# Optimization experiments

Hardware: AMD Instinct MI355X
Metric: run time of the kernel (lower is better)

## Reference

```python
import jax, jax.numpy as jnp
import numpy as np

B, N, IN_DIM, HID, EMB, E = 64, 2048, 128, 256, 64, 4194304
TOTAL = B * N


def _init(key, shape, fan_in):
    return jax.random.normal(key, shape, jnp.float32) / np.sqrt(fan_in).astype(np.float32)


def setup_inputs() -> dict:
    key = jax.random.key(0)
    ks = jax.random.split(key, 9)
    x = jax.random.normal(ks[0], (TOTAL, IN_DIM), jnp.float32)
    src = jax.random.randint(ks[1], (E,), 0, TOTAL)
    dst = jax.random.randint(ks[2], (E,), 0, TOTAL)
    return {
        "x": x,
        "src": src,
        "dst": dst,
        "num_nodes": TOTAL,
        "nodes_per_graph": N,
        "w_lin": _init(ks[3], (IN_DIM, HID), IN_DIM),
        "b_lin": jnp.zeros((HID,), jnp.float32),
        "w_c0": _init(ks[4], (HID, HID), HID),
        "b_c0": jnp.zeros((HID,), jnp.float32),
        "w_c1": _init(ks[5], (HID, HID), HID),
        "b_c1": jnp.zeros((HID,), jnp.float32),
        "w_emb": _init(ks[6], (HID, EMB), HID),
        "b_emb": jnp.zeros((EMB,), jnp.float32),
    }


def reference(x, src, dst, num_nodes, nodes_per_graph,
              w_lin, b_lin, w_c0, b_c0, w_c1, b_c1, w_emb, b_emb):
    # DGL GraphConv norm='both': deg clamped to min 1, symmetric normalization
    ones = jnp.ones(src.shape, x.dtype)
    out_deg = jax.ops.segment_sum(ones, src, num_segments=num_nodes)
    in_deg = jax.ops.segment_sum(ones, dst, num_segments=num_nodes)
    out_norm = jnp.maximum(out_deg, 1.0) ** -0.5  # [num_nodes]
    in_norm = jnp.maximum(in_deg, 1.0) ** -0.5

    def graph_conv(h, W, b):
        hs = h * out_norm[:, None]                                   # pre-norm by out-degree
        agg = jax.ops.segment_sum(hs[src], dst, num_segments=num_nodes)  # SpMM: sum messages
        return (agg * in_norm[:, None]) @ W + b                      # post-norm, then weight

    h = jax.nn.relu(x @ w_lin + b_lin)          # [total, HID]
    h = jax.nn.relu(graph_conv(h, w_c0, b_c0))  # residual=False for agg_style='node'
    h = jax.nn.relu(graph_conv(h, w_c1, b_c1))
    # agent node 0 of each graph in the batch: indices 0, N, 2N, ...
    agent = h[jnp.arange(0, num_nodes, nodes_per_graph)]  # [B, HID]
    return agent @ w_emb + b_emb                          # [B, EMB]
```

## Files before the change

kernel.cpp:

```cpp
#include <hip/hip_runtime.h>
#include <hip/hip_bf16.h>

#define TOTAL_N   131072
#define NEDGE     4194304
#define NPG       2048
#define IN_DIM_K  128
#define HID_K     256
#define EMB_K     64
#define NAGENT    64

#define F1CAP     4096
#define APACK     128
#define BCAP      96

#define G1        256
#define EPB1      (NEDGE / G1)
#define HWORDS    (TOTAL_N / 8)

#define SELB      256
#define EPB       (NEDGE / SELB)


#define ZERO_SPAN 589824

typedef float f32x4 __attribute__((ext_vector_type(4)));
typedef short bf16x8 __attribute__((ext_vector_type(8)));

__device__ inline unsigned short f2bf(float f) {
    unsigned int u = __float_as_uint(f);
    return (unsigned short)((u + 0x7FFFu + ((u >> 16) & 1u)) >> 16);
}

__global__ __launch_bounds__(1024) void k_outdeg_e0(
    const int* __restrict__ src, const int* __restrict__ dst,
    unsigned int* __restrict__ partial,
    int* __restrict__ flag,
    int* __restrict__ e0pack, int* __restrict__ e0cnt)
{
    __shared__ unsigned int hist[HWORDS];
    int t = threadIdx.x;
    #pragma unroll
    for (int i = 0; i < HWORDS / 1024; i++) hist[t + i * 1024] = 0u;
    __syncthreads();

    int ebase = blockIdx.x * EPB1;
    const int4* s4 = (const int4*)(src + ebase);
    const int4* d4 = (const int4*)(dst + ebase);
    #pragma unroll
    for (int i = 0; i < EPB1 / 4096; i++) {
        int4 sv = s4[i * 1024 + t];
        int4 dv = d4[i * 1024 + t];
        int ss[4] = {sv.x, sv.y, sv.z, sv.w};
        int dd[4] = {dv.x, dv.y, dv.z, dv.w};
        #pragma unroll
        for (int j = 0; j < 4; j++) {
            int s = ss[j], d = dd[j];
            atomicAdd(&hist[s >> 3], 1u << ((s & 7) * 4));
            if ((d & (NPG - 1)) == 0) {
                flag[s] = 1;
                int a = d >> 11;
                int slot = atomicAdd(&e0cnt[a], 1);
                if (slot < APACK) e0pack[a * APACK + slot] = s;
            }
        }
    }
    __syncthreads();
    unsigned int* pout = partial + blockIdx.x * HWORDS;
    #pragma unroll
    for (int i = 0; i < HWORDS / 1024; i++) pout[t + i * 1024] = hist[t + i * 1024];
}

__global__ __launch_bounds__(1024) void k_auxred(
    const int* __restrict__ flag, int* __restrict__ loc,
    int* __restrict__ counters, unsigned long long* __restrict__ bitmap,
    const unsigned int* __restrict__ partial, unsigned int* __restrict__ out_deg,
    const float* __restrict__ wlin, unsigned short* __restrict__ wswz)
{
    int b = blockIdx.x;
    int t = threadIdx.x;
    if (b < 128) {
        __shared__ int cnt, gbase;
        if (t == 0) cnt = 0;
        __syncthreads();
        int v = b * 1024 + t;
        int f = flag[v];
        unsigned long long m = __ballot(f != 0);
        if ((t & 63) == 0) bitmap[v >> 6] = m;
        int p = -1;
        if (f) p = atomicAdd(&cnt, 1);
        __syncthreads();
        if (t == 0) gbase = cnt ? atomicAdd(&counters[1], cnt) : 0;
        __syncthreads();
        int l = -1;
        if (p >= 0) { int id = gbase + p; if (id < F1CAP) l = id; }
        loc[v] = l;
    } else if (b < 256) {
        __shared__ unsigned int redE[8][128], redO[8][128];
        int wl = t & 127, gs = t >> 7;
        int w = (b - 128) * 128 + wl;
        unsigned int accE = 0, accO = 0;
        #pragma unroll 8
        for (int i = 0; i < 32; i++) {
            unsigned int v = partial[(gs * 32 + i) * HWORDS + w];
            accE += v & 0x0F0F0F0Fu;
            accO += (v >> 4) & 0x0F0F0F0Fu;
        }
        redE[gs][wl] = accE;
        redO[gs][wl] = accO;
        __syncthreads();
        if (gs == 0) {
            unsigned int sE = 0, sO = 0;
            #pragma unroll
            for (int j = 0; j < 8; j++) { sE += redE[j][wl]; sO += redO[j][wl]; }
            uint4 lo = make_uint4(sE & 255u, sO & 255u, (sE >> 8) & 255u, (sO >> 8) & 255u);
            uint4 hi = make_uint4((sE >> 16) & 255u, (sO >> 16) & 255u, (sE >> 24) & 255u, (sO >> 24) & 255u);
            ((uint4*)(out_deg + 8 * w))[0] = lo;
            ((uint4*)(out_deg + 8 * w))[1] = hi;
        }
    } else {
        int g = (b - 256) * 1024 + t;
        int lane = g & 63, ct = (g >> 6) & 15, kt = g >> 10;
        int colbase = ct * 16 + (lane & 15);
        int kbase = kt * 32 + (lane >> 4) * 8;
        unsigned short o[8];
        #pragma unroll
        for (int i = 0; i < 8; i++) o[i] = f2bf(wlin[(kbase + i) * HID_K + colbase]);
        *(ushort4*)(wswz + g * 8)     = make_ushort4(o[0], o[1], o[2], o[3]);
        *(ushort4*)(wswz + g * 8 + 4) = make_ushort4(o[4], o[5], o[6], o[7]);
    }
}

__global__ __launch_bounds__(1024) void k_e1_select(
    const int* __restrict__ src, const int* __restrict__ dst,
    const int* __restrict__ loc, const unsigned int* __restrict__ bitmap,
    int* __restrict__ inF1, int* __restrict__ es_bucket)
{
    __shared__ unsigned int bm[TOTAL_N / 32];
    int t = threadIdx.x;
    ((uint4*)bm)[t] = ((const uint4*)bitmap)[t];
    __syncthreads();

    int ebase = blockIdx.x * EPB;
    const int4* d4p = (const int4*)(dst + ebase);
    #pragma unroll
    for (int i = 0; i < EPB / 4096; i++) {
        int4 d4 = d4p[i * 1024 + t];
        int eidx = ebase + (i * 1024 + t) * 4;
        int dd[4] = {d4.x, d4.y, d4.z, d4.w};
        #pragma unroll
        for (int j = 0; j < 4; j++) {
            int d = dd[j];
            if ((bm[d >> 5] >> (d & 31)) & 1u) {
                int l = loc[d];
                if (l >= 0) {
                    int slot = atomicAdd(&inF1[l], 1);
                    if (slot < BCAP) es_bucket[l * BCAP + slot] = src[eidx + j];
                }
            }
        }
    }
}

__global__ __launch_bounds__(256) void k_h0agg(
    const float* __restrict__ x, const unsigned short* __restrict__ wswz,
    const float* __restrict__ blin, const int* __restrict__ es_bucket,
    const unsigned int* __restrict__ out_deg, const int* __restrict__ inF1,
    const int* __restrict__ counters, float* __restrict__ agg1)
{
    __shared__ unsigned short A[32][136];
    __shared__ float escs[32];
    __shared__ int rsrc[32];

    int nF1 = min(counters[1], F1CAP);
    int l = blockIdx.x;
    if (l >= nF1) return;
    int cnt = min(inF1[l], BCAP);
    int t = threadIdx.x;
    int lane = t & 63, wq = t >> 6;
    int cbase = lane & 15, rgrp = (lane >> 4) * 4;

    float bj[4];
    #pragma unroll
    for (int n = 0; n < 4; n++) bj[n] = blin[wq * 64 + n * 16 + cbase];

    float colacc[4] = {0.f, 0.f, 0.f, 0.f};
    int ntile = (cnt + 31) >> 5;

    for (int ti = 0; ti < ntile; ti++) {
        __syncthreads();
        if (t < 32) {
            int r = ti * 32 + t;
            int s = (r < cnt) ? es_bucket[l * BCAP + r] : -1;
            rsrc[t] = s;
            escs[t] = (s >= 0) ? rsqrtf((float)max((int)out_deg[s], 1)) : 0.f;
        }
        __syncthreads();
        #pragma unroll
        for (int i = 0; i < 4; i++) {
            int idx = t + i * 256;
            int r = idx >> 5, q = idx & 31;
            int s = rsrc[r];
            float4 v = make_float4(0.f, 0.f, 0.f, 0.f);
            if (s >= 0) v = ((const float4*)(x + (long long)s * IN_DIM_K))[q];
            ushort4 h;
            h.x = f2bf(v.x); h.y = f2bf(v.y); h.z = f2bf(v.z); h.w = f2bf(v.w);
            *(ushort4*)&A[r][q * 4] = h;
        }
        __syncthreads();

        f32x4 acc[2][4];
        #pragma unroll
        for (int m = 0; m < 2; m++)
            #pragma unroll
            for (int n = 0; n < 4; n++) acc[m][n] = (f32x4){0.f, 0.f, 0.f, 0.f};

        const unsigned short* Ab = &A[0][0];
        #pragma unroll
        for (int kt = 0; kt < 4; kt++) {
            bf16x8 a0 = *(const bf16x8*)(Ab + ((lane & 15) * 136 + kt * 32 + (lane >> 4) * 8));
            bf16x8 a1 = *(const bf16x8*)(Ab + (((lane & 15) + 16) * 136 + kt * 32 + (lane >> 4) * 8));
            #pragma unroll
            for (int n = 0; n < 4; n++) {
                bf16x8 bf = *(const bf16x8*)(wswz + ((kt * 16 + wq * 4 + n) * 64 + lane) * 8);
                acc[0][n] = __builtin_amdgcn_mfma_f32_16x16x32_bf16(a0, bf, acc[0][n], 0, 0, 0);
                acc[1][n] = __builtin_amdgcn_mfma_f32_16x16x32_bf16(a1, bf, acc[1][n], 0, 0, 0);
            }
        }

        #pragma unroll
        for (int n = 0; n < 4; n++) {
            float part = 0.f;
            #pragma unroll
            for (int m = 0; m < 2; m++)
                #pragma unroll
                for (int j = 0; j < 4; j++) {
                    int row = m * 16 + rgrp + j;
                    part += fmaxf(acc[m][n][j] + bj[n], 0.f) * escs[row];
                }
            part += __shfl_xor(part, 16);
            part += __shfl_xor(part, 32);
            colacc[n] += part;
        }
    }

    if (lane < 16) {
        #pragma unroll
        for (int n = 0; n < 4; n++)
            agg1[l * HID_K + wq * 64 + n * 16 + lane] = colacc[n];
    }
}

__global__ __launch_bounds__(256) void k_h1(
    const float* __restrict__ agg1, const float* __restrict__ wc0,
    const float* __restrict__ bc0,
    const int* __restrict__ inF1,
    const int* __restrict__ counters, float* __restrict__ h1)
{
    __shared__ float as[16][HID_K];
    __shared__ float ns[16];

    int nF1 = min(counters[1], F1CAP);
    int base = blockIdx.x * 16;
    if (base >= nF1) return;
    int t = threadIdx.x;

    if (t < 16) {
        int l = base + t;
        ns[t] = (l < nF1) ? rsqrtf((float)max(inF1[l], 1)) : 0.f;
    }
    __syncthreads();

    #pragma unroll
    for (int i = 0; i < 4; i++) {
        int idx = t + i * 256;
        int e = idx >> 6;
        int q = idx & 63;
        int l = base + e;
        float4 v = make_float4(0.f, 0.f, 0.f, 0.f);
        if (l < nF1) v = ((const float4*)(agg1 + (long long)l * HID_K))[q];
        float sc = ns[e];
        v.x *= sc; v.y *= sc; v.z *= sc; v.w *= sc;
        ((float4*)as[e])[q] = v;
    }
    __syncthreads();

    float acc[16];
    #pragma unroll
    for (int e = 0; e < 16; e++) acc[e] = 0.f;

    int j = t;
    for (int k = 0; k < HID_K; k += 4) {
        float w0 = wc0[(k + 0) * HID_K + j];
        float w1 = wc0[(k + 1) * HID_K + j];
        float w2 = wc0[(k + 2) * HID_K + j];
        float w3 = wc0[(k + 3) * HID_K + j];
        #pragma unroll
        for (int e = 0; e < 16; e++) {
            float4 av = *(const float4*)&as[e][k];
            acc[e] = fmaf(av.x, w0, acc[e]);
            acc[e] = fmaf(av.y, w1, acc[e]);
            acc[e] = fmaf(av.z, w2, acc[e]);
            acc[e] = fmaf(av.w, w3, acc[e]);
        }
    }

    float bj = bc0[j];
    #pragma unroll
    for (int e = 0; e < 16; e++) {
        int l = base + e;
        if (l < nF1) h1[l * HID_K + j] = fmaxf(acc[e] + bj, 0.f);
    }
}

__global__ __launch_bounds__(256) void k_final(
    const int* __restrict__ e0pack, const int* __restrict__ e0cnt,
    const int* __restrict__ loc, const unsigned int* __restrict__ out_deg,
    const float* __restrict__ h1,
    const float* __restrict__ wc1, const float* __restrict__ bc1,
    const float* __restrict__ wemb, const float* __restrict__ bemb,
    float* __restrict__ out)
{
    __shared__ float a_s[HID_K];
    __shared__ float h2[HID_K];
    __shared__ int   ls[APACK];
    __shared__ float scs[APACK];
    int a = blockIdx.x;
    int t = threadIdx.x;

    int n0 = e0cnt[a];
    int ne = min(n0, APACK);
    if (t < ne) {
        int s = e0pack[a * APACK + t];
        int l = loc[s];
        ls[t] = l;
        scs[t] = (l >= 0) ? rsqrtf((float)max((int)out_deg[s], 1)) : 0.f;
    }
    __syncthreads();

    float acc = 0.f;
    for (int i = 0; i < ne; i++) {
        int l = ls[i];
        if (l >= 0) acc = fmaf(scs[i], h1[(long long)l * HID_K + t], acc);
    }
    a_s[t] = acc * rsqrtf((float)max(n0, 1));
    __syncthreads();

    float h = 0.f;
    for (int k = 0; k < HID_K; k++)
        h = fmaf(a_s[k], wc1[k * HID_K + t], h);
    h2[t] = fmaxf(h + bc1[t], 0.f);
    __syncthreads();

    if (t < EMB_K) {
        float o = bemb[t];
        for (int k = 0; k < HID_K; k++)
            o = fmaf(h2[k], wemb[k * EMB_K + t], o);
        out[a * EMB_K + t] = o;
    }
}

extern "C" void kernel_launch(void* const* d_in, const int* in_sizes, int n_in,
                              void* d_out, int out_size, void* d_ws, size_t ws_size,
                              hipStream_t stream)
{
    const float* x    = (const float*)d_in[0];
    const int*   src  = (const int*)d_in[1];
    const int*   dst  = (const int*)d_in[2];
    const float* wlin = (const float*)d_in[5];
    const float* blin = (const float*)d_in[6];
    const float* wc0  = (const float*)d_in[7];
    const float* bc0  = (const float*)d_in[8];
    const float* wc1  = (const float*)d_in[9];
    const float* bc1  = (const float*)d_in[10];
    const float* wemb = (const float*)d_in[11];
    const float* bemb = (const float*)d_in[12];
    float* out = (float*)d_out;

    char* ws = (char*)d_ws;
    int*                counters  = (int*)(ws + 0);
    int*                inF1      = (int*)(ws + 1024);
    int*                e0cnt     = (int*)(ws + 17408);
    int*                flag      = (int*)(ws + 65536);
    int*                loc       = (int*)(ws + 589824);
    int*                e0pack    = (int*)(ws + 1114112);
    int*                es_bucket = (int*)(ws + 1146880);
    unsigned int*       out_deg   = (unsigned int*)(ws + 2719744);
    unsigned short*     wswz      = (unsigned short*)(ws + 3244032);
    float*              h1        = (float*)(ws + 3309568);
    float*              agg1      = (float*)(ws + 7503872);
    unsigned int*       partial   = (unsigned int*)(ws + 11698176);
    unsigned long long* bitmap    = (unsigned long long*)(ws + 28475392);

    hipMemsetAsync(ws, 0, ZERO_SPAN, stream);

    k_outdeg_e0<<<G1, 1024, 0, stream>>>(src, dst, partial, flag, e0pack, e0cnt);
    k_auxred<<<260, 1024, 0, stream>>>(flag, loc, counters, bitmap,
                                       partial, out_deg, wlin, wswz);
    k_e1_select<<<SELB, 1024, 0, stream>>>(src, dst, loc,
                                           (const unsigned int*)bitmap,
                                           inF1, es_bucket);
    k_h0agg<<<F1CAP, 256, 0, stream>>>(x, wswz, blin, es_bucket, out_deg,
                                       inF1, counters, agg1);
    k_h1<<<F1CAP / 16, 256, 0, stream>>>(agg1, wc0, bc0, inF1, counters, h1);
    k_final<<<NAGENT, 256, 0, stream>>>(e0pack, e0cnt, loc, out_deg, h1,
                                        wc1, bc1, wemb, bemb, out);
}
```

Before: 119.7 us.

## Fuse h0 aggregation with first GraphConv weight; replace flag array with atomic bitmap

Merges the per-node aggregation kernel and the wc0 matmul kernel into one kernel that handles 8 frontier nodes per block. The normalized aggregates stay in shared memory instead of round-tripping through global memory, and the bf16 weight fragments are held in registers across nodes. Separately, the int flag array is replaced by a bitmap built with atomicOr, which shrinks the memset from about 590KB to about 34KB and removes a ballot pass. The trade-offs are serial work inside each block, a launch of only 512 blocks, and more register pressure from the 16 held fragments.

```diff
diff --git a/kernel.cpp b/kernel.cpp
--- a/kernel.cpp
+++ b/kernel.cpp
@@ -12,6 +12,7 @@
 #define F1CAP     4096
 #define APACK     128
 #define BCAP      96
+#define NL        8
 
 #define G1        256
 #define EPB1      (NEDGE / G1)
@@ -21,7 +22,7 @@
 #define EPB       (NEDGE / SELB)
 
 
-#define ZERO_SPAN 589824
+#define ZERO_SPAN 34048
 
 typedef float f32x4 __attribute__((ext_vector_type(4)));
 typedef short bf16x8 __attribute__((ext_vector_type(8)));
@@ -34,7 +35,7 @@
 __global__ __launch_bounds__(1024) void k_outdeg_e0(
     const int* __restrict__ src, const int* __restrict__ dst,
     unsigned int* __restrict__ partial,
-    int* __restrict__ flag,
+    unsigned int* __restrict__ bitmap,
     int* __restrict__ e0pack, int* __restrict__ e0cnt)
 {
     __shared__ unsigned int hist[HWORDS];
@@ -57,7 +58,7 @@
             int s = ss[j], d = dd[j];
             atomicAdd(&hist[s >> 3], 1u << ((s & 7) * 4));
             if ((d & (NPG - 1)) == 0) {
-                flag[s] = 1;
+                atomicOr(&bitmap[s >> 5], 1u << (s & 31));
                 int a = d >> 11;
                 int slot = atomicAdd(&e0cnt[a], 1);
                 if (slot < APACK) e0pack[a * APACK + slot] = s;
@@ -71,8 +72,8 @@
 }
 
 __global__ __launch_bounds__(1024) void k_auxred(
-    const int* __restrict__ flag, int* __restrict__ loc,
-    int* __restrict__ counters, unsigned long long* __restrict__ bitmap,
+    const unsigned int* __restrict__ bitmap, int* __restrict__ loc,
+    int* __restrict__ counters,
     const unsigned int* __restrict__ partial, unsigned int* __restrict__ out_deg,
     const float* __restrict__ wlin, unsigned short* __restrict__ wswz)
 {
@@ -83,9 +84,7 @@
         if (t == 0) cnt = 0;
         __syncthreads();
         int v = b * 1024 + t;
-        int f = flag[v];
-        unsigned long long m = __ballot(f != 0);
-        if ((t & 63) == 0) bitmap[v >> 6] = m;
+        int f = (bitmap[v >> 5] >> (v & 31)) & 1u;
         int p = -1;
         if (f) p = atomicAdd(&cnt, 1);
         __syncthreads();
@@ -161,133 +160,111 @@
     }
 }
 
-__global__ __launch_bounds__(256) void k_h0agg(
+__global__ __launch_bounds__(256) void k_h0h1(
     const float* __restrict__ x, const unsigned short* __restrict__ wswz,
     const float* __restrict__ blin, const int* __restrict__ es_bucket,
     const unsigned int* __restrict__ out_deg, const int* __restrict__ inF1,
-    const int* __restrict__ counters, float* __restrict__ agg1)
+    const int* __restrict__ counters,
+    const float* __restrict__ wc0, const float* __restrict__ bc0,
+    float* __restrict__ h1)
 {
     __shared__ unsigned short A[32][136];
+    __shared__ float as[NL][HID_K];
     __shared__ float escs[32];
     __shared__ int rsrc[32];
 
     int nF1 = min(counters[1], F1CAP);
-    int l = blockIdx.x;
-    if (l >= nF1) return;
-    int cnt = min(inF1[l], BCAP);
+    int base = blockIdx.x * NL;
+    if (base >= nF1) return;
     int t = threadIdx.x;
     int lane = t & 63, wq = t >> 6;
     int cbase = lane & 15, rgrp = (lane >> 4) * 4;
 
+    bf16x8 bfrag[4][4];
+    #pragma unroll
+    for (int kt = 0; kt < 4; kt++)
+        #pragma unroll
+        for (int n = 0; n < 4; n++)
+            bfrag[kt][n] = *(const bf16x8*)(wswz + ((kt * 16 + wq * 4 + n) * 64 + lane) * 8);
+
     float bj[4];
     #pragma unroll
     for (int n = 0; n < 4; n++) bj[n] = blin[wq * 64 + n * 16 + cbase];
 
-    float colacc[4] = {0.f, 0.f, 0.f, 0.f};
-    int ntile = (cnt + 31) >> 5;
-
-    for (int ti = 0; ti < ntile; ti++) {
-        __syncthreads();
-        if (t < 32) {
-            int r = ti * 32 + t;
-            int s = (r < cnt) ? es_bucket[l * BCAP + r] : -1;
-            rsrc[t] = s;
-            escs[t] = (s >= 0) ? rsqrtf((float)max((int)out_deg[s], 1)) : 0.f;
-        }
-        __syncthreads();
-        #pragma unroll
-        for (int i = 0; i < 4; i++) {
-            int idx = t + i * 256;
-            int r = idx >> 5, q = idx & 31;
-            int s = rsrc[r];
-            float4 v = make_float4(0.f, 0.f, 0.f, 0.f);
-            if (s >= 0) v = ((const float4*)(x + (long long)s * IN_DIM_K))[q];
-            ushort4 h;
-            h.x = f2bf(v.x); h.y = f2bf(v.y); h.z = f2bf(v.z); h.w = f2bf(v.w);
-            *(ushort4*)&A[r][q * 4] = h;
-        }
-        __syncthreads();
-
-        f32x4 acc[2][4];
-        #pragma unroll
-        for (int m = 0; m < 2; m++)
-            #pragma unroll
-            for (int n = 0; n < 4; n++) acc[m][n] = (f32x4){0.f, 0.f, 0.f, 0.f};
-
-        const unsigned short* Ab = &A[0][0];
-        #pragma unroll
-        for (int kt = 0; kt < 4; kt++) {
-            bf16x8 a0 = *(const bf16x8*)(Ab + ((lane & 15) * 136 + kt * 32 + (lane >> 4) * 8));
-            bf16x8 a1 = *(const bf16x8*)(Ab + (((lane & 15) + 16) * 136 + kt * 32 + (lane >> 4) * 8));
-            #pragma unroll
-            for (int n = 0; n < 4; n++) {
-                bf16x8 bf = *(const bf16x8*)(wswz + ((kt * 16 + wq * 4 + n) * 64 + lane) * 8);
-                acc[0][n] = __builtin_amdgcn_mfma_f32_16x16x32_bf16(a0, bf, acc[0][n], 0, 0, 0);
-                acc[1][n] = __builtin_amdgcn_mfma_f32_16x16x32_bf16(a1, bf, acc[1][n], 0, 0, 0);
-            }
-        }
-
-        #pragma unroll
-        for (int n = 0; n < 4; n++) {
-            float part = 0.f;
+    for (int r = 0; r < NL; r++) {
+        int l = base + r;
+        int cnt = (l < nF1) ? min(inF1[l], BCAP) : 0;
+        float colacc[4] = {0.f, 0.f, 0.f, 0.f};
+        int ntile = (cnt + 31) >> 5;
+
+        for (int ti = 0; ti < ntile; ti++) {
+            __syncthreads();
+            if (t < 32) {
+                int rr = ti * 32 + t;
+                int s = (rr < cnt) ? es_bucket[l * BCAP + rr] : -1;
+                rsrc[t] = s;
+                escs[t] = (s >= 0) ? rsqrtf((float)max((int)out_deg[s], 1)) : 0.f;
+            }
+            __syncthreads();
+            #pragma unroll
+            for (int i = 0; i < 4; i++) {
+                int idx = t + i * 256;
+                int rr = idx >> 5, q = idx & 31;
+                int s = rsrc[rr];
+                float4 v = make_float4(0.f, 0.f, 0.f, 0.f);
+                if (s >= 0) v = ((const float4*)(x + (long long)s * IN_DIM_K))[q];
+                ushort4 h;
+                h.x = f2bf(v.x); h.y = f2bf(v.y); h.z = f2bf(v.z); h.w = f2bf(v.w);
+                *(ushort4*)&A[rr][q * 4] = h;
+            }
+            __syncthreads();
+
+            f32x4 acc[2][4];
             #pragma unroll
             for (int m = 0; m < 2; m++)
                 #pragma unroll
-                for (int j = 0; j < 4; j++) {
-                    int row = m * 16 + rgrp + j;
-                    part += fmaxf(acc[m][n][j] + bj[n], 0.f) * escs[row];
+                for (int n = 0; n < 4; n++) acc[m][n] = (f32x4){0.f, 0.f, 0.f, 0.f};
+
+            const unsigned short* Ab = &A[0][0];
+            #pragma unroll
+            for (int kt = 0; kt < 4; kt++) {
+                bf16x8 a0 = *(const bf16x8*)(Ab + ((lane & 15) * 136 + kt * 32 + (lane >> 4) * 8));
+                bf16x8 a1 = *(const bf16x8*)(Ab + (((lane & 15) + 16) * 136 + kt * 32 + (lane >> 4) * 8));
+                #pragma unroll
+                for (int n = 0; n < 4; n++) {
+                    acc[0][n] = __builtin_amdgcn_mfma_f32_16x16x32_bf16(a0, bfrag[kt][n], acc[0][n], 0, 0, 0);
+                    acc[1][n] = __builtin_amdgcn_mfma_f32_16x16x32_bf16(a1, bfrag[kt][n], acc[1][n], 0, 0, 0);
                 }
-            part += __shfl_xor(part, 16);
-            part += __shfl_xor(part, 32);
-            colacc[n] += part;
-        }
-    }
-
-    if (lane < 16) {
-        #pragma unroll
-        for (int n = 0; n < 4; n++)
-            agg1[l * HID_K + wq * 64 + n * 16 + lane] = colacc[n];
-    }
-}
-
-__global__ __launch_bounds__(256) void k_h1(
-    const float* __restrict__ agg1, const float* __restrict__ wc0,
-    const float* __restrict__ bc0,
-    const int* __restrict__ inF1,
-    const int* __restrict__ counters, float* __restrict__ h1)
-{
-    __shared__ float as[16][HID_K];
-    __shared__ float ns[16];
-
-    int nF1 = min(counters[1], F1CAP);
-    int base = blockIdx.x * 16;
-    if (base >= nF1) return;
-    int t = threadIdx.x;
-
-    if (t < 16) {
-        int l = base + t;
-        ns[t] = (l < nF1) ? rsqrtf((float)max(inF1[l], 1)) : 0.f;
-    }
-    __syncthreads();
-
-    #pragma unroll
-    for (int i = 0; i < 4; i++) {
-        int idx = t + i * 256;
-        int e = idx >> 6;
-        int q = idx & 63;
-        int l = base + e;
-        float4 v = make_float4(0.f, 0.f, 0.f, 0.f);
-        if (l < nF1) v = ((const float4*)(agg1 + (long long)l * HID_K))[q];
-        float sc = ns[e];
-        v.x *= sc; v.y *= sc; v.z *= sc; v.w *= sc;
-        ((float4*)as[e])[q] = v;
-    }
-    __syncthreads();
-
-    float acc[16];
-    #pragma unroll
-    for (int e = 0; e < 16; e++) acc[e] = 0.f;
-
+            }
+
+            #pragma unroll
+            for (int n = 0; n < 4; n++) {
+                float part = 0.f;
+                #pragma unroll
+                for (int m = 0; m < 2; m++)
+                    #pragma unroll
+                    for (int j = 0; j < 4; j++) {
+                        int row = m * 16 + rgrp + j;
+                        part += fmaxf(acc[m][n][j] + bj[n], 0.f) * escs[row];
+                    }
+                part += __shfl_xor(part, 16);
+                part += __shfl_xor(part, 32);
+                colacc[n] += part;
+            }
+        }
+
+        float ns = (l < nF1) ? rsqrtf((float)max(inF1[l], 1)) : 0.f;
+        if (lane < 16) {
+            #pragma unroll
+            for (int n = 0; n < 4; n++)
+                as[r][wq * 64 + n * 16 + lane] = colacc[n] * ns;
+        }
+    }
+    __syncthreads();
+
+    float acc8[NL];
+    #pragma unroll
+    for (int e = 0; e < NL; e++) acc8[e] = 0.f;
     int j = t;
     for (int k = 0; k < HID_K; k += 4) {
         float w0 = wc0[(k + 0) * HID_K + j];
@@ -295,20 +272,19 @@
         float w2 = wc0[(k + 2) * HID_K + j];
         float w3 = wc0[(k + 3) * HID_K + j];
         #pragma unroll
-        for (int e = 0; e < 16; e++) {
+        for (int e = 0; e < NL; e++) {
             float4 av = *(const float4*)&as[e][k];
-            acc[e] = fmaf(av.x, w0, acc[e]);
-            acc[e] = fmaf(av.y, w1, acc[e]);
-            acc[e] = fmaf(av.z, w2, acc[e]);
-            acc[e] = fmaf(av.w, w3, acc[e]);
-        }
-    }
-
-    float bj = bc0[j];
-    #pragma unroll
-    for (int e = 0; e < 16; e++) {
+            acc8[e] = fmaf(av.x, w0, acc8[e]);
+            acc8[e] = fmaf(av.y, w1, acc8[e]);
+            acc8[e] = fmaf(av.z, w2, acc8[e]);
+            acc8[e] = fmaf(av.w, w3, acc8[e]);
+        }
+    }
+    float bcj = bc0[j];
+    #pragma unroll
+    for (int e = 0; e < NL; e++) {
         int l = base + e;
-        if (l < nF1) h1[l * HID_K + j] = fmaxf(acc[e] + bj, 0.f);
+        if (l < nF1) h1[(long long)l * HID_K + j] = fmaxf(acc8[e] + bcj, 0.f);
     }
 }
 
@@ -377,31 +353,27 @@
     float* out = (float*)d_out;
 
     char* ws = (char*)d_ws;
-    int*                counters  = (int*)(ws + 0);
-    int*                inF1      = (int*)(ws + 1024);
-    int*                e0cnt     = (int*)(ws + 17408);
-    int*                flag      = (int*)(ws + 65536);
-    int*                loc       = (int*)(ws + 589824);
-    int*                e0pack    = (int*)(ws + 1114112);
-    int*                es_bucket = (int*)(ws + 1146880);
-    unsigned int*       out_deg   = (unsigned int*)(ws + 2719744);
-    unsigned short*     wswz      = (unsigned short*)(ws + 3244032);
-    float*              h1        = (float*)(ws + 3309568);
-    float*              agg1      = (float*)(ws + 7503872);
-    unsigned int*       partial   = (unsigned int*)(ws + 11698176);
-    unsigned long long* bitmap    = (unsigned long long*)(ws + 28475392);
+    int*            counters  = (int*)(ws + 0);
+    int*            inF1      = (int*)(ws + 1024);
+    int*            e0cnt     = (int*)(ws + 17408);
+    unsigned int*   bitmap    = (unsigned int*)(ws + 17664);
+    int*            loc       = (int*)(ws + 65536);
+    int*            e0pack    = (int*)(ws + 589824);
+    int*            es_bucket = (int*)(ws + 622592);
+    unsigned int*   out_deg   = (unsigned int*)(ws + 2195456);
+    unsigned short* wswz      = (unsigned short*)(ws + 2719744);
+    float*          h1        = (float*)(ws + 2785280);
+    unsigned int*   partial   = (unsigned int*)(ws + 6979584);
 
     hipMemsetAsync(ws, 0, ZERO_SPAN, stream);
 
-    k_outdeg_e0<<<G1, 1024, 0, stream>>>(src, dst, partial, flag, e0pack, e0cnt);
-    k_auxred<<<260, 1024, 0, stream>>>(flag, loc, counters, bitmap,
+    k_outdeg_e0<<<G1, 1024, 0, stream>>>(src, dst, partial, bitmap, e0pack, e0cnt);
+    k_auxred<<<260, 1024, 0, stream>>>(bitmap, loc, counters,
                                        partial, out_deg, wlin, wswz);
-    k_e1_select<<<SELB, 1024, 0, stream>>>(src, dst, loc,
-                                           (const unsigned int*)bitmap,
+    k_e1_select<<<SELB, 1024, 0, stream>>>(src, dst, loc, bitmap,
                                            inF1, es_bucket);
-    k_h0agg<<<F1CAP, 256, 0, stream>>>(x, wswz, blin, es_bucket, out_deg,
-                                       inF1, counters, agg1);
-    k_h1<<<F1CAP / 16, 256, 0, stream>>>(agg1, wc0, bc0, inF1, counters, h1);
+    k_h0h1<<<F1CAP / NL, 256, 0, stream>>>(x, wswz, blin, es_bucket, out_deg,
+                                           inF1, counters, wc0, bc0, h1);
     k_final<<<NAGENT, 256, 0, stream>>>(e0pack, e0cnt, loc, out_deg, h1,
                                         wc1, bc1, wemb, bemb, out);
 }
```

Measured after the change: 118.3 us. No clear change (-1.2%).

## Replace flag array with atomic bitmap and gather all tiles up front in h0agg

Applied to the files above, without the earlier changes.

The per-node int flag array is replaced by a 16 KB bitmap that k_outdeg_e0 sets with atomicOr. This shrinks the memset from about 576 KB to about 33 KB and removes the ballot pass in k_auxred. In k_h0agg, all up to three 32-row tiles of x are gathered into shared memory in one phase before the MFMA loop, which removes the per-tile syncs and lets more gather loads be in flight at once. The cost is global atomics on the bitmap and about three times the shared memory per block, which may lower occupancy.

```diff
diff --git a/kernel.cpp b/kernel.cpp
--- a/kernel.cpp
+++ b/kernel.cpp
@@ -21,7 +21,7 @@
 #define EPB       (NEDGE / SELB)
 
 
-#define ZERO_SPAN 589824
+#define ZERO_SPAN 34048
 
 typedef float f32x4 __attribute__((ext_vector_type(4)));
 typedef short bf16x8 __attribute__((ext_vector_type(8)));
@@ -34,7 +34,7 @@
 __global__ __launch_bounds__(1024) void k_outdeg_e0(
     const int* __restrict__ src, const int* __restrict__ dst,
     unsigned int* __restrict__ partial,
-    int* __restrict__ flag,
+    unsigned int* __restrict__ bitmap,
     int* __restrict__ e0pack, int* __restrict__ e0cnt)
 {
     __shared__ unsigned int hist[HWORDS];
@@ -57,7 +57,7 @@
             int s = ss[j], d = dd[j];
             atomicAdd(&hist[s >> 3], 1u << ((s & 7) * 4));
             if ((d & (NPG - 1)) == 0) {
-                flag[s] = 1;
+                atomicOr(&bitmap[s >> 5], 1u << (s & 31));
                 int a = d >> 11;
                 int slot = atomicAdd(&e0cnt[a], 1);
                 if (slot < APACK) e0pack[a * APACK + slot] = s;
@@ -71,8 +71,8 @@
 }
 
 __global__ __launch_bounds__(1024) void k_auxred(
-    const int* __restrict__ flag, int* __restrict__ loc,
-    int* __restrict__ counters, unsigned long long* __restrict__ bitmap,
+    const unsigned int* __restrict__ bitmap, int* __restrict__ loc,
+    int* __restrict__ counters,
     const unsigned int* __restrict__ partial, unsigned int* __restrict__ out_deg,
     const float* __restrict__ wlin, unsigned short* __restrict__ wswz)
 {
@@ -83,9 +83,7 @@
         if (t == 0) cnt = 0;
         __syncthreads();
         int v = b * 1024 + t;
-        int f = flag[v];
-        unsigned long long m = __ballot(f != 0);
-        if ((t & 63) == 0) bitmap[v >> 6] = m;
+        int f = (bitmap[v >> 5] >> (v & 31)) & 1u;
         int p = -1;
         if (f) p = atomicAdd(&cnt, 1);
         __syncthreads();
@@ -167,54 +165,52 @@
     const unsigned int* __restrict__ out_deg, const int* __restrict__ inF1,
     const int* __restrict__ counters, float* __restrict__ agg1)
 {
-    __shared__ unsigned short A[32][136];
-    __shared__ float escs[32];
-    __shared__ int rsrc[32];
+    __shared__ unsigned short A[3 * 32][136];
+    __shared__ float escs[3 * 32];
+    __shared__ int rsrc[3 * 32];
 
     int nF1 = min(counters[1], F1CAP);
     int l = blockIdx.x;
     if (l >= nF1) return;
     int cnt = min(inF1[l], BCAP);
+    int ntile = (cnt + 31) >> 5;
     int t = threadIdx.x;
     int lane = t & 63, wq = t >> 6;
     int cbase = lane & 15, rgrp = (lane >> 4) * 4;
 
+    if (t < 96) {
+        int s = (t < cnt) ? es_bucket[l * BCAP + t] : -1;
+        rsrc[t] = s;
+        escs[t] = (s >= 0) ? rsqrtf((float)max((int)out_deg[s], 1)) : 0.f;
+    }
+    __syncthreads();
+
+    int nslots = (ntile * 32) * 32;
+    for (int idx = t; idx < nslots; idx += 256) {
+        int r = idx >> 5, q = idx & 31;
+        int s = rsrc[r];
+        float4 v = make_float4(0.f, 0.f, 0.f, 0.f);
+        if (s >= 0) v = ((const float4*)(x + (long long)s * IN_DIM_K))[q];
+        ushort4 h;
+        h.x = f2bf(v.x); h.y = f2bf(v.y); h.z = f2bf(v.z); h.w = f2bf(v.w);
+        *(ushort4*)&A[r][q * 4] = h;
+    }
+    __syncthreads();
+
     float bj[4];
     #pragma unroll
     for (int n = 0; n < 4; n++) bj[n] = blin[wq * 64 + n * 16 + cbase];
 
     float colacc[4] = {0.f, 0.f, 0.f, 0.f};
-    int ntile = (cnt + 31) >> 5;
 
     for (int ti = 0; ti < ntile; ti++) {
-        __syncthreads();
-        if (t < 32) {
-            int r = ti * 32 + t;
-            int s = (r < cnt) ? es_bucket[l * BCAP + r] : -1;
-            rsrc[t] = s;
-            escs[t] = (s >= 0) ? rsqrtf((float)max((int)out_deg[s], 1)) : 0.f;
-        }
-        __syncthreads();
-        #pragma unroll
-        for (int i = 0; i < 4; i++) {
-            int idx = t + i * 256;
-            int r = idx >> 5, q = idx & 31;
-            int s = rsrc[r];
-            float4 v = make_float4(0.f, 0.f, 0.f, 0.f);
-            if (s >= 0) v = ((const float4*)(x + (long long)s * IN_DIM_K))[q];
-            ushort4 h;
-            h.x = f2bf(v.x); h.y = f2bf(v.y); h.z = f2bf(v.z); h.w = f2bf(v.w);
-            *(ushort4*)&A[r][q * 4] = h;
-        }
-        __syncthreads();
-
         f32x4 acc[2][4];
         #pragma unroll
         for (int m = 0; m < 2; m++)
             #pragma unroll
             for (int n = 0; n < 4; n++) acc[m][n] = (f32x4){0.f, 0.f, 0.f, 0.f};
 
-        const unsigned short* Ab = &A[0][0];
+        const unsigned short* Ab = &A[ti * 32][0];
         #pragma unroll
         for (int kt = 0; kt < 4; kt++) {
             bf16x8 a0 = *(const bf16x8*)(Ab + ((lane & 15) * 136 + kt * 32 + (lane >> 4) * 8));
@@ -235,7 +231,7 @@
                 #pragma unroll
                 for (int j = 0; j < 4; j++) {
                     int row = m * 16 + rgrp + j;
-                    part += fmaxf(acc[m][n][j] + bj[n], 0.f) * escs[row];
+                    part += fmaxf(acc[m][n][j] + bj[n], 0.f) * escs[ti * 32 + row];
                 }
             part += __shfl_xor(part, 16);
             part += __shfl_xor(part, 32);
@@ -246,7 +242,7 @@
     if (lane < 16) {
         #pragma unroll
         for (int n = 0; n < 4; n++)
-            agg1[l * HID_K + wq * 64 + n * 16 + lane] = colacc[n];
+            agg1[(long long)l * HID_K + wq * 64 + n * 16 + lane] = colacc[n];
     }
 }
 
@@ -308,7 +304,7 @@
     #pragma unroll
     for (int e = 0; e < 16; e++) {
         int l = base + e;
-        if (l < nF1) h1[l * HID_K + j] = fmaxf(acc[e] + bj, 0.f);
+        if (l < nF1) h1[(long long)l * HID_K + j] = fmaxf(acc[e] + bj, 0.f);
     }
 }
 
@@ -377,27 +373,25 @@
     float* out = (float*)d_out;
 
     char* ws = (char*)d_ws;
-    int*                counters  = (int*)(ws + 0);
-    int*                inF1      = (int*)(ws + 1024);
-    int*                e0cnt     = (int*)(ws + 17408);
-    int*                flag      = (int*)(ws + 65536);
-    int*                loc       = (int*)(ws + 589824);
-    int*                e0pack    = (int*)(ws + 1114112);
-    int*                es_bucket = (int*)(ws + 1146880);
-    unsigned int*       out_deg   = (unsigned int*)(ws + 2719744);
-    unsigned short*     wswz      = (unsigned short*)(ws + 3244032);
-    float*              h1        = (float*)(ws + 3309568);
-    float*              agg1      = (float*)(ws + 7503872);
-    unsigned int*       partial   = (unsigned int*)(ws + 11698176);
-    unsigned long long* bitmap    = (unsigned long long*)(ws + 28475392);
+    int*            counters  = (int*)(ws + 0);
+    int*            inF1      = (int*)(ws + 1024);
+    int*            e0cnt     = (int*)(ws + 17408);
+    unsigned int*   bitmap    = (unsigned int*)(ws + 17664);
+    int*            loc       = (int*)(ws + 65536);
+    int*            e0pack    = (int*)(ws + 589824);
+    int*            es_bucket = (int*)(ws + 622592);
+    unsigned int*   out_deg   = (unsigned int*)(ws + 2195456);
+    unsigned short* wswz      = (unsigned short*)(ws + 2719744);
+    float*          h1        = (float*)(ws + 2785280);
+    float*          agg1      = (float*)(ws + 6979584);
+    unsigned int*   partial   = (unsigned int*)(ws + 11173888);
 
     hipMemsetAsync(ws, 0, ZERO_SPAN, stream);
 
-    k_outdeg_e0<<<G1, 1024, 0, stream>>>(src, dst, partial, flag, e0pack, e0cnt);
-    k_auxred<<<260, 1024, 0, stream>>>(flag, loc, counters, bitmap,
+    k_outdeg_e0<<<G1, 1024, 0, stream>>>(src, dst, partial, bitmap, e0pack, e0cnt);
+    k_auxred<<<260, 1024, 0, stream>>>(bitmap, loc, counters,
                                        partial, out_deg, wlin, wswz);
-    k_e1_select<<<SELB, 1024, 0, stream>>>(src, dst, loc,
-                                           (const unsigned int*)bitmap,
+    k_e1_select<<<SELB, 1024, 0, stream>>>(src, dst, loc, bitmap,
                                            inF1, es_bucket);
     k_h0agg<<<F1CAP, 256, 0, stream>>>(x, wswz, blin, es_bucket, out_deg,
                                        inF1, counters, agg1);
```

Result: faster. 117.0 us (median of 2 runs) (-2.2%).
